# Optimization experiments

Measured on AMD Instinct MI355X. Metric: run time of the kernel, lower is better.

## Reference

```python
import jax, jax.numpy as jnp
import numpy as np

EPS = 1e-12  # tf.nn.l2_normalize epsilon

def _l2_normalize(x, axis):
    sq = jnp.sum(jnp.square(x), axis=axis, keepdims=True)
    return x * jax.lax.rsqrt(jnp.maximum(sq, EPS))

def setup_inputs() -> dict:
    key = jax.random.key(0)
    k1, k2 = jax.random.split(key)
    B, C, CLS = 8192, 512, 32000
    inputs = jax.random.normal(k1, (B, C), dtype=jnp.float32)
    # glorot_uniform for shape (C, CLS)
    limit = np.sqrt(6.0 / (C + CLS)).astype(np.float32)
    w = jax.random.uniform(k2, (C, CLS), dtype=jnp.float32, minval=-limit, maxval=limit)
    return {"inputs": inputs, "w": w}

def reference(inputs, w):
    # x: [B, C] l2-normalized over channel; w: [C, CLS] l2-normalized over channel.
    # The original broadcast-multiply-reduce over the channel axis == matmul.
    x = _l2_normalize(inputs, axis=-1)
    wn = _l2_normalize(w, axis=0)
    return jnp.einsum('bc,ck->bk', x, wn)  # [B, CLS] cosine similarities
```

## Files before the change

### kernel.cpp

```cpp
#include <hip/hip_runtime.h>
#include <hip/hip_bf16.h>
#include <stdint.h>

#define M_DIM 8192
#define K_DIM 512
#define N_DIM 32000

typedef short bf16x8 __attribute__((ext_vector_type(8)));
typedef float f32x4 __attribute__((ext_vector_type(4)));
typedef unsigned short u16;

__device__ __forceinline__ u16 f2bf(float f) {
  union { float f; uint32_t u; } v; v.f = f;
  uint32_t r = (v.u + 0x7fffu + ((v.u >> 16) & 1u)) >> 16;
  return (u16)r;
}

__global__ void k_zero(float* __restrict__ cn) {
  cn[blockIdx.x * 256 + threadIdx.x] = 0.f;
}

__global__ void k_xnorm(const float* __restrict__ x, u16* __restrict__ xn) {
  int row = (blockIdx.x * blockDim.x + threadIdx.x) >> 6;
  int lane = threadIdx.x & 63;
  const float4* rp = (const float4*)(x + (size_t)row * K_DIM);
  float4 a = rp[lane];
  float4 b = rp[lane + 64];
  float s = a.x*a.x + a.y*a.y + a.z*a.z + a.w*a.w
          + b.x*b.x + b.y*b.y + b.z*b.z + b.w*b.w;
#pragma unroll
  for (int off = 32; off > 0; off >>= 1) s += __shfl_xor(s, off, 64);
  float r = rsqrtf(fmaxf(s, 1e-12f));
  ushort4 o0 = make_ushort4(f2bf(a.x*r), f2bf(a.y*r), f2bf(a.z*r), f2bf(a.w*r));
  ushort4 o1 = make_ushort4(f2bf(b.x*r), f2bf(b.y*r), f2bf(b.z*r), f2bf(b.w*r));
  ushort4* dst = (ushort4*)(xn + (size_t)row * K_DIM);
  dst[lane] = o0;
  dst[lane + 64] = o1;
}

__global__ void k_wtrans(const float* __restrict__ w, float* __restrict__ cn,
                         u16* __restrict__ wT) {
  __shared__ u16 tile[64][68];
  int c0 = blockIdx.x * 64;
  int r0 = blockIdx.y * 64;
  int tc = threadIdx.x & 63;
  int tw = threadIdx.x >> 6;
  float s = 0.f;
#pragma unroll
  for (int i = 0; i < 16; ++i) {
    int r = i * 4 + tw;
    float v = w[(size_t)(r0 + r) * N_DIM + c0 + tc];
    s = fmaf(v, v, s);
    tile[tc][r] = f2bf(v);
  }
  atomicAdd(&cn[c0 + tc], s);
  __syncthreads();
  int cc = threadIdx.x >> 4;
  int rr = (threadIdx.x & 15) * 4;
#pragma unroll
  for (int i = 0; i < 4; ++i) {
    int c = cc + i * 16;
    ushort4 v = *(const ushort4*)&tile[c][rr];
    *(ushort4*)(wT + (size_t)(c0 + c) * K_DIM + r0 + rr) = v;
  }
}

__global__ __launch_bounds__(512, 2) void k_gemm(const u16* __restrict__ A,
                                                 const u16* __restrict__ Bt,
                                                 const float* __restrict__ cn,
                                                 float* __restrict__ C) {
  __shared__ u16 sm[65536];

  int bid = blockIdx.x;
  bid = (bid & 7) * 500 + (bid >> 3);
  const int bm = bid / 125;
  const int bn = bid % 125;

  const int tid = threadIdx.x;
  const int lane = tid & 63;
  const int w = tid >> 6;
  const int wr = w >> 2;
  const int wc = w & 3;
  const int la = lane & 15;
  const int lk = lane >> 4;
  const int swz = lk ^ ((la >> 1) & 3);
  const int aoff = (wr * 128 + la) * 32 + swz * 8;
  const int boff = (wc * 64 + la) * 32 + swz * 8;

  const int sgswz = ((tid & 3) ^ ((tid >> 3) & 3)) * 8;
  const u16* agp = A  + (size_t)(bm * 256 + (tid >> 2)) * K_DIM + sgswz;
  const u16* bgp = Bt + (size_t)(bn * 256 + (tid >> 2)) * K_DIM + sgswz;
  const int d0 = tid * 8;

#define GLLA(koff, eoff)                                                          \
  __builtin_amdgcn_global_load_lds(                                              \
      (const __attribute__((address_space(1))) void*)(agp + (koff)),             \
      (__attribute__((address_space(3))) void*)&sm[(eoff)], 16, 0, 0)
#define GLLB(koff, eoff)                                                          \
  __builtin_amdgcn_global_load_lds(                                              \
      (const __attribute__((address_space(1))) void*)(bgp + (koff)),             \
      (__attribute__((address_space(3))) void*)&sm[(eoff)], 16, 0, 0)
#define STAGE_A(t, h, s)                                                          \
  { GLLA((t)*64 + (h)*32,           (s)*8192 + d0);                               \
    GLLA((t)*64 + (h)*32 + 65536,   (s)*8192 + 4096 + d0); }
#define STAGE_B(t, h, s)                                                          \
  { GLLB((t)*64 + (h)*32,           32768 + (s)*8192 + d0);                       \
    GLLB((t)*64 + (h)*32 + 65536,   32768 + (s)*8192 + 4096 + d0); }

  f32x4 acc[8][4] = {};

  STAGE_A(0, 0, 0); STAGE_B(0, 0, 0);
  STAGE_A(0, 1, 1); STAGE_B(0, 1, 1);
  STAGE_A(1, 0, 2); STAGE_B(1, 0, 2);
  asm volatile("s_waitcnt vmcnt(8)" ::: "memory");
  __builtin_amdgcn_s_barrier();
  __builtin_amdgcn_sched_barrier(0);

#pragma unroll
  for (int kt = 0; kt < 8; ++kt) {
    const int sA0 = (2 * kt) & 3;
    const int sA1 = (2 * kt + 1) & 3;
    const int sT1 = (2 * kt + 3) & 3;
    const int sT2 = (2 * kt + 4) & 3;
    const int t1 = (kt + 1 < 8) ? kt + 1 : 7;
    const int t2 = (kt + 2 < 8) ? kt + 2 : 7;

    bf16x8 bfr[4], af[4];

    STAGE_A(t1, 1, sT1);
#pragma unroll
    for (int n = 0; n < 4; ++n)
      bfr[n] = *(const bf16x8*)&sm[32768 + sA0 * 8192 + boff + n * 512];
#pragma unroll
    for (int m = 0; m < 4; ++m)
      af[m] = *(const bf16x8*)&sm[sA0 * 8192 + aoff + m * 512];
    __builtin_amdgcn_s_barrier();
    asm volatile("s_waitcnt lgkmcnt(0)" ::: "memory");
    __builtin_amdgcn_sched_barrier(0);
    __builtin_amdgcn_s_setprio(1);
#pragma unroll
    for (int m = 0; m < 4; ++m)
#pragma unroll
      for (int n = 0; n < 4; ++n)
        acc[m][n] = __builtin_amdgcn_mfma_f32_16x16x32_bf16(af[m], bfr[n], acc[m][n], 0, 0, 0);
    __builtin_amdgcn_s_setprio(0);
    __builtin_amdgcn_s_barrier();
    __builtin_amdgcn_sched_barrier(0);

    STAGE_B(t1, 1, sT1);
#pragma unroll
    for (int m = 0; m < 4; ++m)
      af[m] = *(const bf16x8*)&sm[sA0 * 8192 + aoff + (4 + m) * 512];
    asm volatile("s_waitcnt vmcnt(8)" ::: "memory");
    __builtin_amdgcn_s_barrier();
    asm volatile("s_waitcnt lgkmcnt(0)" ::: "memory");
    __builtin_amdgcn_sched_barrier(0);
    __builtin_amdgcn_s_setprio(1);
#pragma unroll
    for (int m = 0; m < 4; ++m)
#pragma unroll
      for (int n = 0; n < 4; ++n)
        acc[4 + m][n] = __builtin_amdgcn_mfma_f32_16x16x32_bf16(af[m], bfr[n], acc[4 + m][n], 0, 0, 0);
    __builtin_amdgcn_s_setprio(0);
    __builtin_amdgcn_s_barrier();
    __builtin_amdgcn_sched_barrier(0);

    STAGE_A(t2, 0, sT2);
#pragma unroll
    for (int n = 0; n < 4; ++n)
      bfr[n] = *(const bf16x8*)&sm[32768 + sA1 * 8192 + boff + n * 512];
#pragma unroll
    for (int m = 0; m < 4; ++m)
      af[m] = *(const bf16x8*)&sm[sA1 * 8192 + aoff + m * 512];
    __builtin_amdgcn_s_barrier();
    asm volatile("s_waitcnt lgkmcnt(0)" ::: "memory");
    __builtin_amdgcn_sched_barrier(0);
    __builtin_amdgcn_s_setprio(1);
#pragma unroll
    for (int m = 0; m < 4; ++m)
#pragma unroll
      for (int n = 0; n < 4; ++n)
        acc[m][n] = __builtin_amdgcn_mfma_f32_16x16x32_bf16(af[m], bfr[n], acc[m][n], 0, 0, 0);
    __builtin_amdgcn_s_setprio(0);
    __builtin_amdgcn_s_barrier();
    __builtin_amdgcn_sched_barrier(0);

    STAGE_B(t2, 0, sT2);
#pragma unroll
    for (int m = 0; m < 4; ++m)
      af[m] = *(const bf16x8*)&sm[sA1 * 8192 + aoff + (4 + m) * 512];
    asm volatile("s_waitcnt vmcnt(8)" ::: "memory");
    __builtin_amdgcn_s_barrier();
    asm volatile("s_waitcnt lgkmcnt(0)" ::: "memory");
    __builtin_amdgcn_sched_barrier(0);
    __builtin_amdgcn_s_setprio(1);
#pragma unroll
    for (int m = 0; m < 4; ++m)
#pragma unroll
      for (int n = 0; n < 4; ++n)
        acc[4 + m][n] = __builtin_amdgcn_mfma_f32_16x16x32_bf16(af[m], bfr[n], acc[4 + m][n], 0, 0, 0);
    __builtin_amdgcn_s_setprio(0);
    __builtin_amdgcn_s_barrier();
    __builtin_amdgcn_sched_barrier(0);
  }

  asm volatile("s_waitcnt vmcnt(0)" ::: "memory");
  const size_t crow0 = (size_t)bm * 256 + wr * 128 + lk * 4;
  const int ccol0 = bn * 256 + wc * 64 + la;
  float rs[4];
#pragma unroll
  for (int n = 0; n < 4; ++n)
    rs[n] = rsqrtf(fmaxf(cn[ccol0 + n * 16], 1e-12f));
#pragma unroll
  for (int m = 0; m < 8; ++m)
#pragma unroll
    for (int j = 0; j < 4; ++j) {
      float* cp = C + (crow0 + m * 16 + j) * N_DIM + ccol0;
#pragma unroll
      for (int n = 0; n < 4; ++n)
        __builtin_nontemporal_store(acc[m][n][j] * rs[n], cp + n * 16);
    }
#undef GLLA
#undef GLLB
#undef STAGE_A
#undef STAGE_B
}

extern "C" void kernel_launch(void* const* d_in, const int* in_sizes, int n_in,
                              void* d_out, int out_size, void* d_ws, size_t ws_size,
                              hipStream_t stream) {
  const float* x = (const float*)d_in[0];
  const float* w = (const float*)d_in[1];
  float* out = (float*)d_out;

  char* ws = (char*)d_ws;
  float* cn = (float*)ws;
  u16* xn = (u16*)(ws + 131072);
  u16* wT = (u16*)(ws + 131072 + (size_t)M_DIM * K_DIM * 2);

  k_zero<<<N_DIM / 256, 256, 0, stream>>>(cn);
  k_xnorm<<<M_DIM / 4, 256, 0, stream>>>(x, xn);
  k_wtrans<<<dim3(N_DIM / 64, K_DIM / 64), 256, 0, stream>>>(w, cn, wT);
  k_gemm<<<(M_DIM / 256) * (N_DIM / 256), 512, 0, stream>>>(xn, wT, cn, out);
}
```

Before: 433.2 us.

## Make GEMM persistent with cross-tile prefetch of next tile's K stages

The GEMM launches a fixed grid of 256 blocks instead of one block per 256x256 tile. Each block walks tiles with a stride of 256 and keeps the same swizzled tile order. In the last K iterations it issues the LDS staging loads for the next tile's first stages, so those loads overlap the current tile's epilogue stores. It also drops the explicit sched_barrier and lgkmcnt waits. The intent is to remove launch and tail overhead and hide the pipeline refill between tiles. The cost is only one block per CU (launch bounds allow two), so epilogue stores no longer overlap another block's MFMA work, and 4000 tiles split unevenly across 256 blocks.

```diff
diff --git a/kernel.cpp b/kernel.cpp
--- a/kernel.cpp
+++ b/kernel.cpp
@@ -5,6 +5,8 @@
 #define M_DIM 8192
 #define K_DIM 512
 #define N_DIM 32000
+#define NTILES 4000
+#define NBLK 256
 
 typedef short bf16x8 __attribute__((ext_vector_type(8)));
 typedef float f32x4 __attribute__((ext_vector_type(4)));
@@ -71,11 +73,7 @@
                                                  float* __restrict__ C) {
   __shared__ u16 sm[65536];
 
-  int bid = blockIdx.x;
-  bid = (bid & 7) * 500 + (bid >> 3);
-  const int bm = bid / 125;
-  const int bn = bid % 125;
-
+  const int b = blockIdx.x;
   const int tid = threadIdx.x;
   const int lane = tid & 63;
   const int w = tid >> 6;
@@ -88,140 +86,146 @@
   const int boff = (wc * 64 + la) * 32 + swz * 8;
 
   const int sgswz = ((tid & 3) ^ ((tid >> 3) & 3)) * 8;
-  const u16* agp = A  + (size_t)(bm * 256 + (tid >> 2)) * K_DIM + sgswz;
-  const u16* bgp = Bt + (size_t)(bn * 256 + (tid >> 2)) * K_DIM + sgswz;
+  const int srow = tid >> 2;
   const int d0 = tid * 8;
 
-#define GLLA(koff, eoff)                                                          \
+#define GLL(p, eoff)                                                              \
   __builtin_amdgcn_global_load_lds(                                              \
-      (const __attribute__((address_space(1))) void*)(agp + (koff)),             \
+      (const __attribute__((address_space(1))) void*)(p),                        \
       (__attribute__((address_space(3))) void*)&sm[(eoff)], 16, 0, 0)
-#define GLLB(koff, eoff)                                                          \
-  __builtin_amdgcn_global_load_lds(                                              \
-      (const __attribute__((address_space(1))) void*)(bgp + (koff)),             \
-      (__attribute__((address_space(3))) void*)&sm[(eoff)], 16, 0, 0)
-#define STAGE_A(t, h, s)                                                          \
-  { GLLA((t)*64 + (h)*32,           (s)*8192 + d0);                               \
-    GLLA((t)*64 + (h)*32 + 65536,   (s)*8192 + 4096 + d0); }
-#define STAGE_B(t, h, s)                                                          \
-  { GLLB((t)*64 + (h)*32,           32768 + (s)*8192 + d0);                       \
-    GLLB((t)*64 + (h)*32 + 65536,   32768 + (s)*8192 + 4096 + d0); }
+#define STAGE_A(p, s) { GLL((p), (s)*8192 + d0); GLL((p) + 65536, (s)*8192 + 4096 + d0); }
+#define STAGE_B(p, s) { GLL((p), 32768 + (s)*8192 + d0); GLL((p) + 65536, 32768 + (s)*8192 + 4096 + d0); }
+
+  int seq = b;
+  int bid = (seq & 7) * 500 + (seq >> 3);
+  int bm = bid / 125, bn = bid % 125;
+  const u16* ag = A  + (size_t)(bm * 256 + srow) * K_DIM + sgswz;
+  const u16* bg = Bt + (size_t)(bn * 256 + srow) * K_DIM + sgswz;
 
   f32x4 acc[8][4] = {};
 
-  STAGE_A(0, 0, 0); STAGE_B(0, 0, 0);
-  STAGE_A(0, 1, 1); STAGE_B(0, 1, 1);
-  STAGE_A(1, 0, 2); STAGE_B(1, 0, 2);
+  STAGE_A(ag, 0);       STAGE_B(bg, 0);
+  STAGE_A(ag + 32, 1);  STAGE_B(bg + 32, 1);
+  STAGE_A(ag + 64, 2);  STAGE_B(bg + 64, 2);
   asm volatile("s_waitcnt vmcnt(8)" ::: "memory");
   __builtin_amdgcn_s_barrier();
-  __builtin_amdgcn_sched_barrier(0);
-
-#pragma unroll
-  for (int kt = 0; kt < 8; ++kt) {
-    const int sA0 = (2 * kt) & 3;
-    const int sA1 = (2 * kt + 1) & 3;
-    const int sT1 = (2 * kt + 3) & 3;
-    const int sT2 = (2 * kt + 4) & 3;
-    const int t1 = (kt + 1 < 8) ? kt + 1 : 7;
-    const int t2 = (kt + 2 < 8) ? kt + 2 : 7;
-
-    bf16x8 bfr[4], af[4];
-
-    STAGE_A(t1, 1, sT1);
-#pragma unroll
-    for (int n = 0; n < 4; ++n)
-      bfr[n] = *(const bf16x8*)&sm[32768 + sA0 * 8192 + boff + n * 512];
-#pragma unroll
-    for (int m = 0; m < 4; ++m)
-      af[m] = *(const bf16x8*)&sm[sA0 * 8192 + aoff + m * 512];
-    __builtin_amdgcn_s_barrier();
-    asm volatile("s_waitcnt lgkmcnt(0)" ::: "memory");
-    __builtin_amdgcn_sched_barrier(0);
-    __builtin_amdgcn_s_setprio(1);
-#pragma unroll
-    for (int m = 0; m < 4; ++m)
+
+  for (int ti = 0;; ++ti) {
+    const int seqn = seq + NBLK;
+    const bool last = (seqn >= NTILES);
+    int bmn = bm, bnn = bn;
+    if (!last) {
+      int bidn = (seqn & 7) * 500 + (seqn >> 3);
+      bmn = bidn / 125; bnn = bidn % 125;
+    }
+    const u16* agn = A  + (size_t)(bmn * 256 + srow) * K_DIM + sgswz;
+    const u16* bgn = Bt + (size_t)(bnn * 256 + srow) * K_DIM + sgswz;
+
+#pragma unroll
+    for (int kt = 0; kt < 8; ++kt) {
+      const int sA0 = (2 * kt) & 3;
+      const int sA1 = (2 * kt + 1) & 3;
+      const int sT1 = (2 * kt + 3) & 3;
+      const int sT2 = (2 * kt + 4) & 3;
+      const u16* a1 = (kt < 7) ? (ag + (kt + 1) * 64 + 32) : (agn + 32);
+      const u16* b1 = (kt < 7) ? (bg + (kt + 1) * 64 + 32) : (bgn + 32);
+      const u16* a2 = (kt < 6) ? (ag + (kt + 2) * 64) : ((kt == 6) ? agn : (agn + 64));
+      const u16* b2 = (kt < 6) ? (bg + (kt + 2) * 64) : ((kt == 6) ? bgn : (bgn + 64));
+
+      bf16x8 bfr[4], af[4];
+
+      STAGE_A(a1, sT1);
 #pragma unroll
       for (int n = 0; n < 4; ++n)
-        acc[m][n] = __builtin_amdgcn_mfma_f32_16x16x32_bf16(af[m], bfr[n], acc[m][n], 0, 0, 0);
-    __builtin_amdgcn_s_setprio(0);
-    __builtin_amdgcn_s_barrier();
-    __builtin_amdgcn_sched_barrier(0);
-
-    STAGE_B(t1, 1, sT1);
-#pragma unroll
-    for (int m = 0; m < 4; ++m)
-      af[m] = *(const bf16x8*)&sm[sA0 * 8192 + aoff + (4 + m) * 512];
-    asm volatile("s_waitcnt vmcnt(8)" ::: "memory");
-    __builtin_amdgcn_s_barrier();
-    asm volatile("s_waitcnt lgkmcnt(0)" ::: "memory");
-    __builtin_amdgcn_sched_barrier(0);
-    __builtin_amdgcn_s_setprio(1);
-#pragma unroll
-    for (int m = 0; m < 4; ++m)
+        bfr[n] = *(const bf16x8*)&sm[32768 + sA0 * 8192 + boff + n * 512];
+#pragma unroll
+      for (int m = 0; m < 4; ++m)
+        af[m] = *(const bf16x8*)&sm[sA0 * 8192 + aoff + m * 512];
+      __builtin_amdgcn_s_barrier();
+      __builtin_amdgcn_s_setprio(1);
+#pragma unroll
+      for (int m = 0; m < 4; ++m)
+#pragma unroll
+        for (int n = 0; n < 4; ++n)
+          acc[m][n] = __builtin_amdgcn_mfma_f32_16x16x32_bf16(af[m], bfr[n], acc[m][n], 0, 0, 0);
+      __builtin_amdgcn_s_setprio(0);
+      __builtin_amdgcn_s_barrier();
+
+      STAGE_B(b1, sT1);
+#pragma unroll
+      for (int m = 0; m < 4; ++m)
+        af[m] = *(const bf16x8*)&sm[sA0 * 8192 + aoff + (4 + m) * 512];
+      asm volatile("s_waitcnt vmcnt(8)" ::: "memory");
+      __builtin_amdgcn_s_barrier();
+      __builtin_amdgcn_s_setprio(1);
+#pragma unroll
+      for (int m = 0; m < 4; ++m)
+#pragma unroll
+        for (int n = 0; n < 4; ++n)
+          acc[4 + m][n] = __builtin_amdgcn_mfma_f32_16x16x32_bf16(af[m], bfr[n], acc[4 + m][n], 0, 0, 0);
+      __builtin_amdgcn_s_setprio(0);
+      __builtin_amdgcn_s_barrier();
+
+      STAGE_A(a2, sT2);
 #pragma unroll
       for (int n = 0; n < 4; ++n)
-        acc[4 + m][n] = __builtin_amdgcn_mfma_f32_16x16x32_bf16(af[m], bfr[n], acc[4 + m][n], 0, 0, 0);
-    __builtin_amdgcn_s_setprio(0);
-    __builtin_amdgcn_s_barrier();
-    __builtin_amdgcn_sched_barrier(0);
-
-    STAGE_A(t2, 0, sT2);
-#pragma unroll
-    for (int n = 0; n < 4; ++n)
-      bfr[n] = *(const bf16x8*)&sm[32768 + sA1 * 8192 + boff + n * 512];
-#pragma unroll
-    for (int m = 0; m < 4; ++m)
-      af[m] = *(const bf16x8*)&sm[sA1 * 8192 + aoff + m * 512];
-    __builtin_amdgcn_s_barrier();
-    asm volatile("s_waitcnt lgkmcnt(0)" ::: "memory");
-    __builtin_amdgcn_sched_barrier(0);
-    __builtin_amdgcn_s_setprio(1);
-#pragma unroll
-    for (int m = 0; m < 4; ++m)
+        bfr[n] = *(const bf16x8*)&sm[32768 + sA1 * 8192 + boff + n * 512];
+#pragma unroll
+      for (int m = 0; m < 4; ++m)
+        af[m] = *(const bf16x8*)&sm[sA1 * 8192 + aoff + m * 512];
+      __builtin_amdgcn_s_barrier();
+      __builtin_amdgcn_s_setprio(1);
+#pragma unroll
+      for (int m = 0; m < 4; ++m)
+#pragma unroll
+        for (int n = 0; n < 4; ++n)
+          acc[m][n] = __builtin_amdgcn_mfma_f32_16x16x32_bf16(af[m], bfr[n], acc[m][n], 0, 0, 0);
+      __builtin_amdgcn_s_setprio(0);
+      __builtin_amdgcn_s_barrier();
+
+      STAGE_B(b2, sT2);
+#pragma unroll
+      for (int m = 0; m < 4; ++m)
+        af[m] = *(const bf16x8*)&sm[sA1 * 8192 + aoff + (4 + m) * 512];
+      asm volatile("s_waitcnt vmcnt(8)" ::: "memory");
+      __builtin_amdgcn_s_barrier();
+      __builtin_amdgcn_s_setprio(1);
+#pragma unroll
+      for (int m = 0; m < 4; ++m)
+#pragma unroll
+        for (int n = 0; n < 4; ++n)
+          acc[4 + m][n] = __builtin_amdgcn_mfma_f32_16x16x32_bf16(af[m], bfr[n], acc[4 + m][n], 0, 0, 0);
+      __builtin_amdgcn_s_setprio(0);
+      __builtin_amdgcn_s_barrier();
+    }
+
+    {
+      const size_t crow0 = (size_t)bm * 256 + wr * 128 + lk * 4;
+      const int ccol0 = bn * 256 + wc * 64 + la;
+      float rs[4];
 #pragma unroll
       for (int n = 0; n < 4; ++n)
-        acc[m][n] = __builtin_amdgcn_mfma_f32_16x16x32_bf16(af[m], bfr[n], acc[m][n], 0, 0, 0);
-    __builtin_amdgcn_s_setprio(0);
-    __builtin_amdgcn_s_barrier();
-    __builtin_amdgcn_sched_barrier(0);
-
-    STAGE_B(t2, 0, sT2);
-#pragma unroll
-    for (int m = 0; m < 4; ++m)
-      af[m] = *(const bf16x8*)&sm[sA1 * 8192 + aoff + (4 + m) * 512];
-    asm volatile("s_waitcnt vmcnt(8)" ::: "memory");
-    __builtin_amdgcn_s_barrier();
-    asm volatile("s_waitcnt lgkmcnt(0)" ::: "memory");
-    __builtin_amdgcn_sched_barrier(0);
-    __builtin_amdgcn_s_setprio(1);
-#pragma unroll
-    for (int m = 0; m < 4; ++m)
-#pragma unroll
-      for (int n = 0; n < 4; ++n)
-        acc[4 + m][n] = __builtin_amdgcn_mfma_f32_16x16x32_bf16(af[m], bfr[n], acc[4 + m][n], 0, 0, 0);
-    __builtin_amdgcn_s_setprio(0);
-    __builtin_amdgcn_s_barrier();
-    __builtin_amdgcn_sched_barrier(0);
+        rs[n] = rsqrtf(fmaxf(cn[ccol0 + n * 16], 1e-12f));
+#pragma unroll
+      for (int m = 0; m < 8; ++m)
+#pragma unroll
+        for (int j = 0; j < 4; ++j) {
+          float* cp = C + (crow0 + m * 16 + j) * N_DIM + ccol0;
+#pragma unroll
+          for (int n = 0; n < 4; ++n)
+            __builtin_nontemporal_store(acc[m][n][j] * rs[n], cp + n * 16);
+        }
+#pragma unroll
+      for (int m = 0; m < 8; ++m)
+#pragma unroll
+        for (int n = 0; n < 4; ++n)
+          acc[m][n] = (f32x4){0.f, 0.f, 0.f, 0.f};
+    }
+
+    if (last) break;
+    seq = seqn; bm = bmn; bn = bnn; ag = agn; bg = bgn;
   }
-
-  asm volatile("s_waitcnt vmcnt(0)" ::: "memory");
-  const size_t crow0 = (size_t)bm * 256 + wr * 128 + lk * 4;
-  const int ccol0 = bn * 256 + wc * 64 + la;
-  float rs[4];
-#pragma unroll
-  for (int n = 0; n < 4; ++n)
-    rs[n] = rsqrtf(fmaxf(cn[ccol0 + n * 16], 1e-12f));
-#pragma unroll
-  for (int m = 0; m < 8; ++m)
-#pragma unroll
-    for (int j = 0; j < 4; ++j) {
-      float* cp = C + (crow0 + m * 16 + j) * N_DIM + ccol0;
-#pragma unroll
-      for (int n = 0; n < 4; ++n)
-        __builtin_nontemporal_store(acc[m][n][j] * rs[n], cp + n * 16);
-    }
-#undef GLLA
-#undef GLLB
+#undef GLL
 #undef STAGE_A
 #undef STAGE_B
 }
@@ -241,5 +245,5 @@
   k_zero<<<N_DIM / 256, 256, 0, stream>>>(cn);
   k_xnorm<<<M_DIM / 4, 256, 0, stream>>>(x, xn);
   k_wtrans<<<dim3(N_DIM / 64, K_DIM / 64), 256, 0, stream>>>(w, cn, wT);
-  k_gemm<<<(M_DIM / 256) * (N_DIM / 256), 512, 0, stream>>>(xn, wT, cn, out);
-}
+  k_gemm<<<NBLK, 512, 0, stream>>>(xn, wT, cn, out);
+}
```

After: 420.9 us. 2.8% less time.
